# Kernel optimization log

Hardware: AMD Instinct MI355X
Metric: run time of the kernel (lower is better)

Reference implementation:

```python
import jax, jax.numpy as jnp
import numpy as np

T = 1024          # num tokens
H = 2048          # hidden_size
NH = 16           # attention heads
NKV = 4           # kv heads (GQA)
HD = 128          # head_dim
E = 32            # num routed experts
K = 4             # top_k
I = 1024          # moe_intermediate_size
NS = 1            # num_shared_experts
EPS = 1e-6
THETA = 600000.0  # rope base
SCALE = HD ** -0.5


def rmsnorm(x, w):
    return x * jax.lax.rsqrt(jnp.mean(x * x, axis=-1, keepdims=True) + EPS) * w


def rope(x, positions):
    # x: [T, n_heads, HD], neox-style rotation on full head_dim
    half = HD // 2
    inv_freq = 1.0 / (THETA ** (jnp.arange(half, dtype=jnp.float32) / half))
    ang = positions.astype(jnp.float32)[:, None] * inv_freq        # [T, half]
    cos = jnp.cos(ang)[:, None, :]
    sin = jnp.sin(ang)[:, None, :]
    x1, x2 = x[..., :half], x[..., half:]
    return jnp.concatenate([x1 * cos - x2 * sin, x1 * sin + x2 * cos], axis=-1)


def setup_inputs() -> dict:
    key = jax.random.key(0)
    ks = jax.random.split(key, 10)
    s = 0.02
    return {
        "hidden_states": jax.random.normal(ks[0], (T, H), dtype=jnp.float32),
        "positions": jnp.arange(T, dtype=jnp.int32),
        "w_rms1": jnp.ones((H,), jnp.float32),
        "w_rms2": jnp.ones((H,), jnp.float32),
        "w_qkv": jax.random.normal(ks[1], ((NH + 2 * NKV) * HD, H), jnp.float32) * s,
        "w_o": jax.random.normal(ks[2], (H, NH * HD), jnp.float32) * s,
        "w_router": jax.random.normal(ks[3], (E, H), jnp.float32) * s,
        "w1": jax.random.normal(ks[4], (E, H, I), jnp.float32) * s,   # expert gate proj
        "w3": jax.random.normal(ks[5], (E, H, I), jnp.float32) * s,   # expert up proj
        "w2": jax.random.normal(ks[6], (E, I, H), jnp.float32) * s,   # expert down proj
        "ws_gate_up": jax.random.normal(ks[7], (2 * I * NS, H), jnp.float32) * s,
        "ws_down": jax.random.normal(ks[8], (H, I * NS), jnp.float32) * s,
    }


def reference(hidden_states, positions, w_rms1, w_rms2, w_qkv, w_o, w_router,
              w1, w3, w2, ws_gate_up, ws_down):
    x = hidden_states
    # ---- attention block ----
    h = rmsnorm(x, w_rms1)
    qkv = h @ w_qkv.T                                   # [T, (NH+2NKV)*HD]
    q = qkv[:, : NH * HD].reshape(T, NH, HD)
    k = qkv[:, NH * HD : (NH + NKV) * HD].reshape(T, NKV, HD)
    v = qkv[:, (NH + NKV) * HD :].reshape(T, NKV, HD)
    q = rope(q, positions)
    k = rope(k, positions)
    rep = NH // NKV
    k = jnp.repeat(k, rep, axis=1)                      # [T, NH, HD]
    v = jnp.repeat(v, rep, axis=1)
    scores = jnp.einsum("thd,shd->hts", q, k) * SCALE   # [NH, T, T]
    causal = jnp.tril(jnp.ones((T, T), dtype=bool))
    scores = jnp.where(causal, scores, -jnp.inf)
    attn = jax.nn.softmax(scores, axis=-1)
    o = jnp.einsum("hts,shd->thd", attn, v).reshape(T, NH * HD)
    x = x + o @ w_o.T                                   # residual
    # ---- MoE block ----
    h2 = rmsnorm(x, w_rms2)
    # router in fp32 (router_dtype default)
    logits = h2.astype(jnp.float32) @ w_router.T        # [T, E]
    probs = jax.nn.softmax(logits, axis=-1)
    topv, topi = jax.lax.top_k(probs, K)                # [T, K]
    topv = topv / jnp.sum(topv, axis=-1, keepdims=True)  # norm_topk_prob
    combine = jnp.zeros((T, E), jnp.float32).at[jnp.arange(T)[:, None], topi].add(topv)
    combine = combine.astype(h2.dtype)                  # routed_scaling_factor = 1.0
    g = jnp.einsum("th,ehi->tei", h2, w1)               # [T, E, I]
    u = jnp.einsum("th,ehi->tei", h2, w3)
    a = jax.nn.silu(g) * u                              # SiluAndMul
    d = jnp.einsum("tei,eih->teh", a, w2)               # [T, E, H]
    routed = jnp.einsum("teh,te->th", d, combine)
    # shared expert MLP
    gu = h2 @ ws_gate_up.T                              # [T, 2*I*NS]
    gs, us = gu[:, : I * NS], gu[:, I * NS :]
    shared = (jax.nn.silu(gs) * us) @ ws_down.T
    return x + routed + shared
```

## Files before the change

### kernel.cpp

```cpp
#include <hip/hip_runtime.h>
#include <hip/hip_bf16.h>
#include <math.h>
#include <stdint.h>

#define T_ 1024
#define H_ 2048
#define NH_ 16
#define NKV_ 4
#define HD_ 128
#define E_ 32
#define TOPK_ 4
#define I_ 1024
#define QKVN_ 3072
#define EPS_ 1e-6f
#define THETA_ 600000.0f
#define SCALE_ 0.08838834764831845f

typedef unsigned short u16;
typedef u16 u16x4 __attribute__((ext_vector_type(4)));
typedef u16 u16x8 __attribute__((ext_vector_type(8)));
typedef __bf16 bf16x8 __attribute__((ext_vector_type(8)));
typedef float f32x4 __attribute__((ext_vector_type(4)));

__device__ __forceinline__ u16 f2b(float f) {
  unsigned u = __builtin_bit_cast(unsigned, f);
  u += 0x7FFFu + ((u >> 16) & 1u);
  return (u16)(u >> 16);
}
__device__ __forceinline__ float b2f(u16 x) {
  unsigned u = ((unsigned)x) << 16;
  return __builtin_bit_cast(float, u);
}
__device__ __forceinline__ int s2(int i) { return (i ^ (i >> 2)) & 3; }

__device__ __forceinline__ void gload16(const void* g, void* l) {
  __builtin_amdgcn_global_load_lds(
      reinterpret_cast<const __attribute__((address_space(1))) unsigned int*>(
          reinterpret_cast<uintptr_t>(g)),
      reinterpret_cast<__attribute__((address_space(3))) unsigned int*>(
          reinterpret_cast<uintptr_t>(l)),
      16, 0, 0);
}

template<int EPI, bool GATHER>
__global__ __launch_bounds__(512, 8) void moe_gemm_k(
    const u16* __restrict__ A, const float* __restrict__ B, const float* __restrict__ B2,
    float* __restrict__ O1, float* __restrict__ O2,
    int NW, int lda, int ldb, int K,
    const int* __restrict__ eoff, const int* __restrict__ tpre,
    const int* __restrict__ slots, const float* __restrict__ slotw, long long sBz)
{
  __shared__ u16 As[2][64 * 32];
  __shared__ u16 Bs[2][128 * 32];

  const int idx = blockIdx.x;
  const int t = idx >> 4;
  const int xx = idx & 15;
  if (t >= tpre[E_]) return;
  int lo = 0, hi = E_;
  while (hi - lo > 1) { int mid = (lo + hi) >> 1; if (tpre[mid] <= t) lo = mid; else hi = mid; }
  const int e = lo;
  const int mb = t - tpre[e];
  const int goff = eoff[e];
  const int Mloc = eoff[e + 1] - goff;
  const int m0 = mb * 64;

  const float* Bp;
  float* Op;
  int n0;
  if constexpr (EPI == 0) {
    int wsel = xx >> 3;
    n0 = (xx & 7) * 128;
    Bp = (wsel ? B2 : B) + (long long)e * sBz;
    Op = wsel ? O2 : O1;
  } else {
    n0 = xx * 128;
    Bp = B + (long long)e * sBz;
    Op = O1;
  }
  const u16* Ae = GATHER ? A : (A + (long long)goff * lda);

  const int tid = threadIdx.x;
  const int lane = tid & 63;
  const int wv = tid >> 6;
  const int wm = wv >> 2, wn = wv & 3;
  const int kg = lane >> 4;
  const int cr = lane & 15;

  const u16* Abase = nullptr;
  if (wv < 4) {
    int r = wv * 16 + (lane >> 2);
    int rr = m0 + r;
    if (rr > Mloc - 1) rr = Mloc - 1;
    long long grow = GATHER ? (long long)slots[goff + rr] : (long long)rr;
    Abase = Ae + grow * (long long)lda + (((lane & 3) ^ s2(r)) << 3);
  }

  const int bn = tid & 127;
  const int bkc = tid >> 7;
  const float* Bbase = Bp + (long long)(bkc << 3) * ldb + n0 + bn;
  const int bws = bn * 32 + ((bkc ^ s2(bn)) << 3);

  float br[8];
  auto loadB = [&](int k0) {
    const float* p = Bbase + (long long)k0 * ldb;
    #pragma unroll
    for (int j = 0; j < 8; ++j) br[j] = p[(long long)j * ldb];
  };
  auto writeB = [&](int bf) {
    u16x8 o;
    #pragma unroll
    for (int j = 0; j < 8; ++j) o[j] = f2b(br[j]);
    *(u16x8*)(&Bs[bf][bws]) = o;
  };
  auto stageA = [&](int bf, int k0) {
    if (wv < 4) gload16(Abase + k0, &As[bf][wv * 512]);
  };

  f32x4 acc[2][2];
  #pragma unroll
  for (int m = 0; m < 2; ++m)
    #pragma unroll
    for (int n = 0; n < 2; ++n)
      acc[m][n] = f32x4{0.f, 0.f, 0.f, 0.f};

  int aoff[2], boff[2];
  #pragma unroll
  for (int m = 0; m < 2; ++m) {
    int r = wm * 32 + m * 16 + cr;
    aoff[m] = r * 32 + ((kg ^ s2(r)) << 3);
  }
  #pragma unroll
  for (int n = 0; n < 2; ++n) {
    int c = wn * 32 + n * 16 + cr;
    boff[n] = c * 32 + ((kg ^ s2(c)) << 3);
  }

  loadB(0);
  stageA(0, 0);
  writeB(0);
  __syncthreads();

  int buf = 0;
  for (int ks = 0; ks < K; ks += 32) {
    bool more = (ks + 32) < K;
    if (more) { loadB(ks + 32); stageA(buf ^ 1, ks + 32); }
    const u16* Ap = &As[buf][0];
    const u16* Bq = &Bs[buf][0];
    bf16x8 af[2], bfr[2];
    #pragma unroll
    for (int m = 0; m < 2; ++m)
      af[m] = __builtin_bit_cast(bf16x8, *(const u16x8*)(Ap + aoff[m]));
    #pragma unroll
    for (int n = 0; n < 2; ++n)
      bfr[n] = __builtin_bit_cast(bf16x8, *(const u16x8*)(Bq + boff[n]));
    #pragma unroll
    for (int m = 0; m < 2; ++m)
      #pragma unroll
      for (int n = 0; n < 2; ++n)
        acc[m][n] = __builtin_amdgcn_mfma_f32_16x16x32_bf16(af[m], bfr[n], acc[m][n], 0, 0, 0);
    if (more) writeB(buf ^ 1);
    __syncthreads();
    buf ^= 1;
  }

  const int rq = lane >> 4;
  #pragma unroll
  for (int m = 0; m < 2; ++m) {
    #pragma unroll
    for (int j = 0; j < 4; ++j) {
      int row = m0 + wm * 32 + m * 16 + rq * 4 + j;
      if (row >= Mloc) continue;
      if constexpr (EPI == 0) {
        float* dst = Op + (long long)(goff + row) * NW;
        #pragma unroll
        for (int n = 0; n < 2; ++n) {
          int col = n0 + wn * 32 + n * 16 + cr;
          dst[col] = acc[m][n][j];
        }
      } else {
        int tok = slots[goff + row];
        float wgt = slotw[goff + row];
        float* dst = Op + (long long)tok * NW;
        #pragma unroll
        for (int n = 0; n < 2; ++n) {
          int col = n0 + wn * 32 + n * 16 + cr;
          atomicAdd(dst + col, wgt * acc[m][n][j]);
        }
      }
    }
  }
}

template<typename TB, int EPI, int CAUSAL>
__global__ __launch_bounds__(512, 8) void dense_gemm_k(
    const u16* __restrict__ A, const TB* __restrict__ B,
    u16* __restrict__ Cb, float* __restrict__ Cf,
    const float* __restrict__ res1, const float* __restrict__ res2,
    int K, int lda, int ldb, int ldc, float alpha,
    long long sAz, long long sBz, long long sCz, int bdivz)
{
  __shared__ u16 As[2][64 * 32];
  __shared__ u16 Bs[2][128 * 32];

  const int m0 = blockIdx.y * 64;
  const int n0 = blockIdx.x * 128;
  if (CAUSAL == 1 && n0 > m0 + 63) return;
  const long long z = blockIdx.z;
  const u16* Ae = A + z * sAz;
  const TB* Be = B + (long long)(z / bdivz) * sBz;
  u16* Cwb = Cb ? Cb + z * sCz : nullptr;

  int kend = K;
  if (CAUSAL == 2) { int ke = m0 + 64; if (ke < kend) kend = ke; }

  const int tid = threadIdx.x;
  const int lane = tid & 63;
  const int wv = tid >> 6;
  const int wm = wv >> 2, wn = wv & 3;

  const u16* Abase = nullptr;
  if (wv < 4) {
    int r = wv * 16 + (lane >> 2);
    Abase = Ae + (long long)(m0 + r) * lda + (((lane & 3) ^ s2(r)) << 3);
  }
  auto stageA = [&](int bf, int k0) {
    if (wv < 4) gload16(Abase + k0, &As[bf][wv * 512]);
  };

  const u16* Bu16base = nullptr;
  const float* Bf32base = nullptr;
  int bws = 0;
  if constexpr (sizeof(TB) == 2) {
    int r = wv * 16 + (lane >> 2);
    Bu16base = (const u16*)Be + (long long)(n0 + r) * ldb + (((lane & 3) ^ s2(r)) << 3);
  } else {
    int bn = tid >> 2, bkq = tid & 3;
    Bf32base = (const float*)Be + (long long)(n0 + bn) * ldb + (bkq << 3);
    bws = bn * 32 + ((bkq ^ s2(bn)) << 3);
  }
  float br[8];
  auto loadB = [&](int k0) {
    const float* p = Bf32base + k0;
    float4 a = *(const float4*)p;
    float4 b = *(const float4*)(p + 4);
    br[0] = a.x; br[1] = a.y; br[2] = a.z; br[3] = a.w;
    br[4] = b.x; br[5] = b.y; br[6] = b.z; br[7] = b.w;
  };
  auto writeB = [&](int bf) {
    u16x8 o;
    #pragma unroll
    for (int j = 0; j < 8; ++j) o[j] = f2b(br[j]);
    *(u16x8*)(&Bs[bf][bws]) = o;
  };
  auto stageBu = [&](int bf, int k0) {
    gload16(Bu16base + k0, &Bs[bf][wv * 512]);
  };

  f32x4 acc[2][2];
  #pragma unroll
  for (int m = 0; m < 2; ++m)
    #pragma unroll
    for (int n = 0; n < 2; ++n)
      acc[m][n] = f32x4{0.f, 0.f, 0.f, 0.f};

  const int kg = lane >> 4;
  const int cr = lane & 15;

  int aoff[2], boff[2];
  #pragma unroll
  for (int m = 0; m < 2; ++m) {
    int r = wm * 32 + m * 16 + cr;
    aoff[m] = r * 32 + ((kg ^ s2(r)) << 3);
  }
  #pragma unroll
  for (int n = 0; n < 2; ++n) {
    int c = wn * 32 + n * 16 + cr;
    boff[n] = c * 32 + ((kg ^ s2(c)) << 3);
  }

  if constexpr (sizeof(TB) == 4) {
    loadB(0); stageA(0, 0); writeB(0);
  } else {
    stageA(0, 0); stageBu(0, 0);
  }
  __syncthreads();

  int buf = 0;
  for (int ks = 0; ks < kend; ks += 32) {
    bool more = (ks + 32) < kend;
    if (more) {
      if constexpr (sizeof(TB) == 4) { loadB(ks + 32); stageA(buf ^ 1, ks + 32); }
      else { stageA(buf ^ 1, ks + 32); stageBu(buf ^ 1, ks + 32); }
    }
    const u16* Ap = &As[buf][0];
    const u16* Bq = &Bs[buf][0];
    bf16x8 af[2], bfr[2];
    #pragma unroll
    for (int m = 0; m < 2; ++m)
      af[m] = __builtin_bit_cast(bf16x8, *(const u16x8*)(Ap + aoff[m]));
    #pragma unroll
    for (int n = 0; n < 2; ++n)
      bfr[n] = __builtin_bit_cast(bf16x8, *(const u16x8*)(Bq + boff[n]));
    #pragma unroll
    for (int m = 0; m < 2; ++m)
      #pragma unroll
      for (int n = 0; n < 2; ++n)
        acc[m][n] = __builtin_amdgcn_mfma_f32_16x16x32_bf16(af[m], bfr[n], acc[m][n], 0, 0, 0);
    if constexpr (sizeof(TB) == 4) { if (more) writeB(buf ^ 1); }
    __syncthreads();
    buf ^= 1;
  }

  const int rq = lane >> 4;
  #pragma unroll
  for (int m = 0; m < 2; ++m) {
    #pragma unroll
    for (int j = 0; j < 4; ++j) {
      int row = m0 + wm * 32 + m * 16 + rq * 4 + j;
      #pragma unroll
      for (int n = 0; n < 2; ++n) {
        int col = n0 + wn * 32 + n * 16 + cr;
        float v = acc[m][n][j];
        long long o = (long long)row * ldc + col;
        if constexpr (EPI == 0) {
          Cwb[o] = f2b(v);
        } else if constexpr (EPI == 1) {
          Cwb[o] = f2b(v * alpha);
        } else if constexpr (EPI == 2) {
          Cf[o] = res1[o] + v;
        } else {
          Cf[o] = res1[o] + res2[o] + v;
        }
      }
    }
  }
}

__global__ __launch_bounds__(256) void vtrans_k(const u16* __restrict__ v_r,
                                                u16* __restrict__ v_t) {
  __shared__ u16 t[64][72];
  int kv = blockIdx.z;
  int s0 = blockIdx.x * 64, d0 = blockIdx.y * 64;
  int tid = threadIdx.x;
  int sr = tid >> 2, dq = (tid & 3) * 16;
  const u16* src = v_r + ((long long)kv * T_ + s0 + sr) * HD_ + d0 + dq;
  *(u16x8*)&t[sr][dq] = *(const u16x8*)src;
  *(u16x8*)&t[sr][dq + 8] = *(const u16x8*)(src + 8);
  __syncthreads();
  int dr = tid >> 2, sq = (tid & 3) * 16;
  u16* dst = v_t + ((long long)kv * HD_ + d0 + dr) * T_ + s0 + sq;
  u16x8 o0, o1;
  #pragma unroll
  for (int j = 0; j < 8; ++j) { o0[j] = t[sq + j][dr]; o1[j] = t[sq + 8 + j][dr]; }
  *(u16x8*)dst = o0;
  *(u16x8*)(dst + 8) = o1;
}

__global__ __launch_bounds__(256) void rmsnorm_k(const float* __restrict__ x,
                                                 const float* __restrict__ w,
                                                 u16* __restrict__ outb,
                                                 float* __restrict__ outf) {
  int t = blockIdx.x;
  int tid = threadIdx.x;
  const float* xr = x + (long long)t * H_;
  float4 a = *(const float4*)(xr + tid * 8);
  float4 b = *(const float4*)(xr + tid * 8 + 4);
  float ss = a.x * a.x + a.y * a.y + a.z * a.z + a.w * a.w +
             b.x * b.x + b.y * b.y + b.z * b.z + b.w * b.w;
  #pragma unroll
  for (int o = 32; o; o >>= 1) ss += __shfl_down(ss, o);
  __shared__ float red[4];
  if ((tid & 63) == 0) red[tid >> 6] = ss;
  __syncthreads();
  float sc = rsqrtf((red[0] + red[1] + red[2] + red[3]) * (1.0f / H_) + EPS_);
  float vo[8] = {a.x, a.y, a.z, a.w, b.x, b.y, b.z, b.w};
  const float* wr = w + tid * 8;
  u16x8 ob;
  #pragma unroll
  for (int q = 0; q < 8; ++q) {
    float val = vo[q] * sc * wr[q];
    ob[q] = f2b(val);
    if (outf) outf[(long long)t * H_ + tid * 8 + q] = val;
  }
  *(u16x8*)(outb + (long long)t * H_ + tid * 8) = ob;
}

__global__ __launch_bounds__(256) void rope_k(const u16* __restrict__ qkv,
                                              const int* __restrict__ pos,
                                              u16* __restrict__ q_r,
                                              u16* __restrict__ k_r,
                                              u16* __restrict__ v_r) {
  int t = blockIdx.x;
  int tid = threadIdx.x;
  float p = (float)pos[t];
  const u16* row = qkv + (long long)t * QKVN_;
  const float cfac = logf(THETA_) * (1.0f / 64.0f);
  #pragma unroll
  for (int it = 0; it < 4; ++it) {
    int item = it * 256 + tid;
    int h = item >> 6, d = item & 63;
    float inv = expf(-cfac * (float)d);
    float ang = p * inv;
    float c = cosf(ang), s = sinf(ang);
    float x1v = b2f(row[h * 128 + d]);
    float x2v = b2f(row[h * 128 + 64 + d]);
    u16* dst = q_r + ((long long)h * T_ + t) * HD_;
    dst[d] = f2b(x1v * c - x2v * s);
    dst[d + 64] = f2b(x1v * s + x2v * c);
  }
  {
    int item = tid;
    int kv = item >> 6, d = item & 63;
    float inv = expf(-cfac * (float)d);
    float ang = p * inv;
    float c = cosf(ang), s = sinf(ang);
    float x1v = b2f(row[NH_ * HD_ + kv * 128 + d]);
    float x2v = b2f(row[NH_ * HD_ + kv * 128 + 64 + d]);
    u16* dst = k_r + ((long long)kv * T_ + t) * HD_;
    dst[d] = f2b(x1v * c - x2v * s);
    dst[d + 64] = f2b(x1v * s + x2v * c);
  }
  #pragma unroll
  for (int it = 0; it < 2; ++it) {
    int item = it * 256 + tid;
    int kv = item >> 7, d = item & 127;
    v_r[((long long)kv * T_ + t) * HD_ + d] = row[(NH_ + NKV_) * HD_ + kv * 128 + d];
  }
}

__global__ __launch_bounds__(64) void softmax_k(u16* __restrict__ P) {
  int r = blockIdx.x;
  int h = r >> 10, i = r & 1023;
  u16* row = P + ((long long)h * T_ + i) * T_;
  int lane = threadIdx.x;
  int n = i + 1;
  float vals[16];
  float mx = -1e30f;
  #pragma unroll
  for (int it = 0; it < 16; ++it) {
    int j = it * 64 + lane;
    float s = (j < n) ? b2f(row[j]) : -1e30f;
    vals[it] = s;
    mx = fmaxf(mx, s);
  }
  #pragma unroll
  for (int o = 32; o; o >>= 1) mx = fmaxf(mx, __shfl_xor(mx, o));
  float sum = 0.f;
  #pragma unroll
  for (int it = 0; it < 16; ++it) {
    int j = it * 64 + lane;
    float e = (j < n) ? __expf(vals[it] - mx) : 0.f;
    vals[it] = e;
    sum += e;
  }
  #pragma unroll
  for (int o = 32; o; o >>= 1) sum += __shfl_xor(sum, o);
  float inv = 1.f / sum;
  #pragma unroll
  for (int it = 0; it < 16; ++it) {
    int j = it * 64 + lane;
    row[j] = f2b(vals[it] * inv);
  }
}

__global__ __launch_bounds__(256) void router2_k(const float* __restrict__ h2,
                                                 const float* __restrict__ wr,
                                                 float* __restrict__ logits) {
  __shared__ float hrow[H_];
  int t = blockIdx.x;
  int tid = threadIdx.x;
  float4 a = *(const float4*)(h2 + (long long)t * H_ + tid * 8);
  float4 b = *(const float4*)(h2 + (long long)t * H_ + tid * 8 + 4);
  *(float4*)&hrow[tid * 8] = a;
  *(float4*)&hrow[tid * 8 + 4] = b;
  __syncthreads();
  int wv = tid >> 6, lane = tid & 63;
  #pragma unroll
  for (int ei = 0; ei < 8; ++ei) {
    int e = wv * 8 + ei;
    const float* wrow = wr + (long long)e * H_;
    float s = 0.f;
    #pragma unroll
    for (int it = 0; it < 8; ++it) {
      int k = it * 256 + lane * 4;
      float4 w4 = *(const float4*)(wrow + k);
      s += hrow[k] * w4.x + hrow[k + 1] * w4.y + hrow[k + 2] * w4.z + hrow[k + 3] * w4.w;
    }
    #pragma unroll
    for (int o = 32; o; o >>= 1) s += __shfl_xor(s, o);
    if (lane == 0) logits[t * E_ + e] = s;
  }
}

__global__ __launch_bounds__(256) void topk_k(const float* __restrict__ logits,
                                              int* __restrict__ topi,
                                              float* __restrict__ topw) {
  int t = blockIdx.x * 256 + threadIdx.x;
  if (t >= T_) return;
  float l[E_];
  #pragma unroll
  for (int e = 0; e < E_; ++e) l[e] = logits[t * E_ + e];
  int sel[TOPK_];
  float sv[TOPK_];
  unsigned used = 0;
  for (int j = 0; j < TOPK_; ++j) {
    float best = -1e30f;
    int bi = 0;
    for (int e = 0; e < E_; ++e) {
      if (used & (1u << e)) continue;
      if (l[e] > best) { best = l[e]; bi = e; }
    }
    used |= 1u << bi;
    sel[j] = bi;
    sv[j] = best;
  }
  float mx = sv[0];
  float s = 0.f;
  #pragma unroll
  for (int j = 0; j < TOPK_; ++j) { sv[j] = __expf(sv[j] - mx); s += sv[j]; }
  float inv = 1.f / s;
  #pragma unroll
  for (int j = 0; j < TOPK_; ++j) {
    topi[t * TOPK_ + j] = sel[j];
    topw[t * TOPK_ + j] = sv[j] * inv;
  }
}

__global__ __launch_bounds__(256) void hist_k(const int* __restrict__ topi, int* __restrict__ cnt) {
  int idx = blockIdx.x * 256 + threadIdx.x;
  if (idx < T_ * TOPK_) atomicAdd(&cnt[topi[idx]], 1);
}

__global__ __launch_bounds__(64) void scan_k(const int* __restrict__ cnt,
                                             int* __restrict__ eoff,
                                             int* __restrict__ cursor,
                                             int* __restrict__ tpre) {
  if (threadIdx.x == 0) {
    int s = 0, tt = 0;
    for (int e = 0; e < E_; ++e) {
      eoff[e] = s; cursor[e] = s; tpre[e] = tt;
      tt += (cnt[e] + 63) >> 6;
      s += cnt[e];
    }
    eoff[E_] = s; tpre[E_] = tt;
  }
}

__global__ __launch_bounds__(256) void scatter_k(const int* __restrict__ topi,
                                                 const float* __restrict__ topw,
                                                 int* __restrict__ cursor,
                                                 int* __restrict__ slots,
                                                 float* __restrict__ slotw) {
  int idx = blockIdx.x * 256 + threadIdx.x;
  if (idx >= T_ * TOPK_) return;
  int e = topi[idx];
  int pos = atomicAdd(&cursor[e], 1);
  slots[pos] = idx >> 2;
  slotw[pos] = topw[idx];
}

__global__ __launch_bounds__(256) void silumul_f_k(const float* __restrict__ g,
                                                   const float* __restrict__ u,
                                                   u16* __restrict__ a) {
  long long idx = ((long long)blockIdx.x * 256 + threadIdx.x) * 8;
  float4 g0 = *(const float4*)(g + idx);
  float4 g1 = *(const float4*)(g + idx + 4);
  float4 u0 = *(const float4*)(u + idx);
  float4 u1 = *(const float4*)(u + idx + 4);
  float gv[8] = {g0.x, g0.y, g0.z, g0.w, g1.x, g1.y, g1.z, g1.w};
  float uv[8] = {u0.x, u0.y, u0.z, u0.w, u1.x, u1.y, u1.z, u1.w};
  u16x8 o;
  #pragma unroll
  for (int q = 0; q < 8; ++q) {
    float x = gv[q];
    float sl = x / (1.f + __expf(-x));
    o[q] = f2b(sl * uv[q]);
  }
  *(u16x8*)(a + idx) = o;
}

__global__ __launch_bounds__(256) void sharedact_k(const u16* __restrict__ gu,
                                                   u16* __restrict__ act) {
  long long idx = ((long long)blockIdx.x * 256 + threadIdx.x) * 8;
  long long t = idx >> 10;
  int i = (int)(idx & 1023);
  const u16* row = gu + t * (2 * I_);
  u16x8 g = *(const u16x8*)(row + i);
  u16x8 u = *(const u16x8*)(row + I_ + i);
  u16x8 o;
  #pragma unroll
  for (int q = 0; q < 8; ++q) {
    float x = b2f(g[q]);
    float y = b2f(u[q]);
    float sl = x / (1.f + __expf(-x));
    o[q] = f2b(sl * y);
  }
  *(u16x8*)(act + t * I_ + i) = o;
}

extern "C" void kernel_launch(void* const* d_in, const int* in_sizes, int n_in,
                              void* d_out, int out_size, void* d_ws, size_t ws_size,
                              hipStream_t stream) {
  const float* x        = (const float*)d_in[0];
  const int* positions  = (const int*)d_in[1];
  const float* w_rms1   = (const float*)d_in[2];
  const float* w_rms2   = (const float*)d_in[3];
  const float* w_qkv    = (const float*)d_in[4];
  const float* w_o      = (const float*)d_in[5];
  const float* w_router = (const float*)d_in[6];
  const float* w1       = (const float*)d_in[7];
  const float* w3       = (const float*)d_in[8];
  const float* w2       = (const float*)d_in[9];
  const float* ws_gu    = (const float*)d_in[10];
  const float* ws_dn    = (const float*)d_in[11];
  float* out = (float*)d_out;

  char* ws = (char*)d_ws;
  size_t off = 0;
  auto alloc = [&](size_t bytes) {
    size_t o = off;
    off = (off + bytes + 255) & ~(size_t)255;
    return (void*)(ws + o);
  };
  u16*  h1b     = (u16*)alloc((size_t)T_ * H_ * 2);
  u16*  qkvb    = (u16*)alloc((size_t)T_ * QKVN_ * 2);
  u16*  q_r     = (u16*)alloc((size_t)NH_ * T_ * HD_ * 2);
  u16*  k_r     = (u16*)alloc((size_t)NKV_ * T_ * HD_ * 2);
  u16*  v_r     = (u16*)alloc((size_t)NKV_ * T_ * HD_ * 2);
  u16*  v_t     = (u16*)alloc((size_t)NKV_ * HD_ * T_ * 2);
  u16*  scoresP = (u16*)alloc((size_t)NH_ * T_ * T_ * 2);
  u16*  o_attn  = (u16*)alloc((size_t)T_ * H_ * 2);
  float* x1     = (float*)alloc((size_t)T_ * H_ * 4);
  float* h2f    = (float*)alloc((size_t)T_ * H_ * 4);
  u16*  h2b     = (u16*)alloc((size_t)T_ * H_ * 2);
  u16*  gub     = (u16*)alloc((size_t)T_ * 2 * I_ * 2);
  u16*  actsh   = (u16*)alloc((size_t)T_ * I_ * 2);
  float* logits = (float*)alloc((size_t)T_ * E_ * 4);
  int*  topi    = (int*)alloc((size_t)T_ * TOPK_ * 4);
  float* topw   = (float*)alloc((size_t)T_ * TOPK_ * 4);
  int*  cnt     = (int*)alloc(E_ * 4);
  int*  eoffp   = (int*)alloc((E_ + 1) * 4);
  int*  cursor  = (int*)alloc(E_ * 4);
  int*  tpre    = (int*)alloc((E_ + 1) * 4);
  int*  slots   = (int*)alloc((size_t)T_ * TOPK_ * 4);
  float* slotw  = (float*)alloc((size_t)T_ * TOPK_ * 4);
  u16*  a_g     = (u16*)alloc((size_t)T_ * TOPK_ * I_ * 2);
  float* routed = (float*)alloc((size_t)T_ * H_ * 4);

  float* g_f32 = (float*)scoresP;
  float* u_f32 = g_f32 + (size_t)T_ * TOPK_ * I_;

  hipMemsetAsync(routed, 0, (size_t)T_ * H_ * 4, stream);
  hipMemsetAsync(cnt, 0, E_ * 4, stream);

  rmsnorm_k<<<T_, 256, 0, stream>>>(x, w_rms1, h1b, nullptr);

  dense_gemm_k<float, 0, 0><<<dim3(24, 16, 1), 512, 0, stream>>>(
      h1b, w_qkv, qkvb, nullptr, nullptr, nullptr,
      H_, H_, H_, QKVN_, 1.f, 0, 0, 0, 1);

  rope_k<<<T_, 256, 0, stream>>>(qkvb, positions, q_r, k_r, v_r);
  vtrans_k<<<dim3(16, 2, 4), 256, 0, stream>>>(v_r, v_t);

  dense_gemm_k<u16, 1, 1><<<dim3(8, 16, NH_), 512, 0, stream>>>(
      q_r, k_r, scoresP, nullptr, nullptr, nullptr,
      HD_, HD_, HD_, T_, SCALE_,
      (long long)T_ * HD_, (long long)T_ * HD_, (long long)T_ * T_, NH_ / NKV_);

  softmax_k<<<NH_ * T_, 64, 0, stream>>>(scoresP);

  dense_gemm_k<u16, 0, 2><<<dim3(1, 16, NH_), 512, 0, stream>>>(
      scoresP, v_t, o_attn, nullptr, nullptr, nullptr,
      T_, T_, T_, H_, 1.f,
      (long long)T_ * T_, (long long)HD_ * T_, (long long)HD_, NH_ / NKV_);

  dense_gemm_k<float, 2, 0><<<dim3(16, 16, 1), 512, 0, stream>>>(
      o_attn, w_o, nullptr, x1, x, nullptr,
      H_, H_, H_, H_, 1.f, 0, 0, 0, 1);

  rmsnorm_k<<<T_, 256, 0, stream>>>(x1, w_rms2, h2b, h2f);

  router2_k<<<T_, 256, 0, stream>>>(h2f, w_router, logits);
  topk_k<<<4, 256, 0, stream>>>(logits, topi, topw);
  hist_k<<<16, 256, 0, stream>>>(topi, cnt);
  scan_k<<<1, 64, 0, stream>>>(cnt, eoffp, cursor, tpre);
  scatter_k<<<16, 256, 0, stream>>>(topi, topw, cursor, slots, slotw);

  moe_gemm_k<0, true><<<1536, 512, 0, stream>>>(
      h2b, w1, w3, g_f32, u_f32,
      I_, H_, I_, H_, eoffp, tpre, slots, nullptr, (long long)H_ * I_);
  silumul_f_k<<<(T_ * TOPK_ * I_) / (256 * 8), 256, 0, stream>>>(g_f32, u_f32, a_g);

  moe_gemm_k<1, false><<<1536, 512, 0, stream>>>(
      a_g, w2, nullptr, routed, nullptr,
      H_, I_, H_, I_, eoffp, tpre, slots, slotw, (long long)I_ * H_);

  dense_gemm_k<float, 0, 0><<<dim3(16, 16, 1), 512, 0, stream>>>(
      h2b, ws_gu, gub, nullptr, nullptr, nullptr,
      H_, H_, H_, 2 * I_, 1.f, 0, 0, 0, 1);
  sharedact_k<<<(T_ * I_) / (256 * 8), 256, 0, stream>>>(gub, actsh);

  dense_gemm_k<float, 4, 0><<<dim3(16, 16, 1), 512, 0, stream>>>(
      actsh, ws_dn, nullptr, out, x1, routed,
      I_, I_, I_, H_, 1.f, 0, 0, 0, 1);
}
```

Baseline: 589.1 us.

## Double MoE GEMM K-tile to 64 with 8-way swizzle and all-warp A staging

```diff
diff --git a/kernel.cpp b/kernel.cpp
--- a/kernel.cpp
+++ b/kernel.cpp
@@ -32,6 +32,7 @@
   return __builtin_bit_cast(float, u);
 }
 __device__ __forceinline__ int s2(int i) { return (i ^ (i >> 2)) & 3; }
+__device__ __forceinline__ int sw3(int i) { return (i ^ (i >> 3)) & 7; }
 
 __device__ __forceinline__ void gload16(const void* g, void* l) {
   __builtin_amdgcn_global_load_lds(
@@ -43,15 +44,15 @@
 }
 
 template<int EPI, bool GATHER>
-__global__ __launch_bounds__(512, 8) void moe_gemm_k(
+__global__ __launch_bounds__(512, 6) void moe_gemm_k(
     const u16* __restrict__ A, const float* __restrict__ B, const float* __restrict__ B2,
     float* __restrict__ O1, float* __restrict__ O2,
     int NW, int lda, int ldb, int K,
     const int* __restrict__ eoff, const int* __restrict__ tpre,
     const int* __restrict__ slots, const float* __restrict__ slotw, long long sBz)
 {
-  __shared__ u16 As[2][64 * 32];
-  __shared__ u16 Bs[2][128 * 32];
+  __shared__ u16 As[2][64 * 64];
+  __shared__ u16 Bs[2][128 * 64];
 
   const int idx = blockIdx.x;
   const int t = idx >> 4;
@@ -87,34 +88,40 @@
   const int kg = lane >> 4;
   const int cr = lane & 15;
 
-  const u16* Abase = nullptr;
-  if (wv < 4) {
-    int r = wv * 16 + (lane >> 2);
+  const u16* Abase;
+  {
+    int r = wv * 8 + (lane >> 3);
     int rr = m0 + r;
     if (rr > Mloc - 1) rr = Mloc - 1;
     long long grow = GATHER ? (long long)slots[goff + rr] : (long long)rr;
-    Abase = Ae + grow * (long long)lda + (((lane & 3) ^ s2(r)) << 3);
-  }
+    Abase = Ae + grow * (long long)lda + (((lane & 7) ^ sw3(r)) << 3);
+  }
+  auto stageA = [&](int bf, int k0) {
+    gload16(Abase + k0, &As[bf][wv * 512]);
+  };
 
   const int bn = tid & 127;
-  const int bkc = tid >> 7;
-  const float* Bbase = Bp + (long long)(bkc << 3) * ldb + n0 + bn;
-  const int bws = bn * 32 + ((bkc ^ s2(bn)) << 3);
-
-  float br[8];
+  const int q = tid >> 7;
+  const float* Bb0 = Bp + (long long)(q << 3) * ldb + n0 + bn;
+  const float* Bb1 = Bp + (long long)((q + 4) << 3) * ldb + n0 + bn;
+  const int bws0 = bn * 64 + (((q)     ^ sw3(bn)) << 3);
+  const int bws1 = bn * 64 + (((q + 4) ^ sw3(bn)) << 3);
+
+  float br[16];
   auto loadB = [&](int k0) {
-    const float* p = Bbase + (long long)k0 * ldb;
-    #pragma unroll
-    for (int j = 0; j < 8; ++j) br[j] = p[(long long)j * ldb];
+    const float* p0 = Bb0 + (long long)k0 * ldb;
+    const float* p1 = Bb1 + (long long)k0 * ldb;
+    #pragma unroll
+    for (int j = 0; j < 8; ++j) br[j] = p0[(long long)j * ldb];
+    #pragma unroll
+    for (int j = 0; j < 8; ++j) br[8 + j] = p1[(long long)j * ldb];
   };
   auto writeB = [&](int bf) {
-    u16x8 o;
-    #pragma unroll
-    for (int j = 0; j < 8; ++j) o[j] = f2b(br[j]);
-    *(u16x8*)(&Bs[bf][bws]) = o;
-  };
-  auto stageA = [&](int bf, int k0) {
-    if (wv < 4) gload16(Abase + k0, &As[bf][wv * 512]);
+    u16x8 o0, o1;
+    #pragma unroll
+    for (int j = 0; j < 8; ++j) { o0[j] = f2b(br[j]); o1[j] = f2b(br[8 + j]); }
+    *(u16x8*)(&Bs[bf][bws0]) = o0;
+    *(u16x8*)(&Bs[bf][bws1]) = o1;
   };
 
   f32x4 acc[2][2];
@@ -124,17 +131,38 @@
     for (int n = 0; n < 2; ++n)
       acc[m][n] = f32x4{0.f, 0.f, 0.f, 0.f};
 
-  int aoff[2], boff[2];
+  int aoff[2], asw[2], boff[2], bsw[2];
   #pragma unroll
   for (int m = 0; m < 2; ++m) {
     int r = wm * 32 + m * 16 + cr;
-    aoff[m] = r * 32 + ((kg ^ s2(r)) << 3);
+    aoff[m] = r * 64; asw[m] = sw3(r);
   }
   #pragma unroll
   for (int n = 0; n < 2; ++n) {
     int c = wn * 32 + n * 16 + cr;
-    boff[n] = c * 32 + ((kg ^ s2(c)) << 3);
-  }
+    boff[n] = c * 64; bsw[n] = sw3(c);
+  }
+
+  auto mfma_step = [&](int bf) {
+    const u16* Ap = &As[bf][0];
+    const u16* Bq = &Bs[bf][0];
+    #pragma unroll
+    for (int sub = 0; sub < 2; ++sub) {
+      int ck = kg + sub * 4;
+      bf16x8 af[2], bfr[2];
+      #pragma unroll
+      for (int m = 0; m < 2; ++m)
+        af[m] = __builtin_bit_cast(bf16x8, *(const u16x8*)(Ap + aoff[m] + ((ck ^ asw[m]) << 3)));
+      #pragma unroll
+      for (int n = 0; n < 2; ++n)
+        bfr[n] = __builtin_bit_cast(bf16x8, *(const u16x8*)(Bq + boff[n] + ((ck ^ bsw[n]) << 3)));
+      #pragma unroll
+      for (int m = 0; m < 2; ++m)
+        #pragma unroll
+        for (int n = 0; n < 2; ++n)
+          acc[m][n] = __builtin_amdgcn_mfma_f32_16x16x32_bf16(af[m], bfr[n], acc[m][n], 0, 0, 0);
+    }
+  };
 
   loadB(0);
   stageA(0, 0);
@@ -142,23 +170,10 @@
   __syncthreads();
 
   int buf = 0;
-  for (int ks = 0; ks < K; ks += 32) {
-    bool more = (ks + 32) < K;
-    if (more) { loadB(ks + 32); stageA(buf ^ 1, ks + 32); }
-    const u16* Ap = &As[buf][0];
-    const u16* Bq = &Bs[buf][0];
-    bf16x8 af[2], bfr[2];
-    #pragma unroll
-    for (int m = 0; m < 2; ++m)
-      af[m] = __builtin_bit_cast(bf16x8, *(const u16x8*)(Ap + aoff[m]));
-    #pragma unroll
-    for (int n = 0; n < 2; ++n)
-      bfr[n] = __builtin_bit_cast(bf16x8, *(const u16x8*)(Bq + boff[n]));
-    #pragma unroll
-    for (int m = 0; m < 2; ++m)
-      #pragma unroll
-      for (int n = 0; n < 2; ++n)
-        acc[m][n] = __builtin_amdgcn_mfma_f32_16x16x32_bf16(af[m], bfr[n], acc[m][n], 0, 0, 0);
+  for (int ks = 0; ks < K; ks += 64) {
+    bool more = (ks + 64) < K;
+    if (more) { loadB(ks + 64); stageA(buf ^ 1, ks + 64); }
+    mfma_step(buf);
     if (more) writeB(buf ^ 1);
     __syncthreads();
     buf ^= 1;
```

Result: slower. 1.317 ms (+123.5%).
